# Optimization experiments

Measured on AMD Instinct MI355X. Metric: run time of the kernel, lower is better.

The kernel has to match this reference:

```python
import jax, jax.numpy as jnp
import numpy as np

N_NODES = 50000
N_EDGES = 1600000
IN_CH = 128
OUT_CH = 64
HEADS = 2
NEG_SLOPE = 0.2


def setup_inputs() -> dict:
    key = jax.random.key(0)
    ks = jax.random.split(key, 9)
    return {
        "x": jax.random.normal(ks[0], (N_NODES, IN_CH), dtype=jnp.float32),
        "embedding": jax.random.normal(ks[1], (N_NODES, OUT_CH), dtype=jnp.float32),
        "lin_w": jax.random.normal(ks[2], (IN_CH, HEADS * OUT_CH), dtype=jnp.float32) * (1.0 / np.sqrt(IN_CH)),
        "att_i": jax.random.normal(ks[3], (HEADS, OUT_CH), dtype=jnp.float32) * 0.1,
        "att_j": jax.random.normal(ks[4], (HEADS, OUT_CH), dtype=jnp.float32) * 0.1,
        "att_em_i": jax.random.normal(ks[5], (HEADS, OUT_CH), dtype=jnp.float32) * 0.1,
        "att_em_j": jax.random.normal(ks[6], (HEADS, OUT_CH), dtype=jnp.float32) * 0.1,
        "edge_src": jax.random.randint(ks[7], (N_EDGES,), 0, N_NODES, dtype=jnp.int64 if jax.config.read("jax_enable_x64") else jnp.int32),
        "edge_dst": jax.random.randint(ks[8], (N_EDGES,), 0, N_NODES, dtype=jnp.int64 if jax.config.read("jax_enable_x64") else jnp.int32),
    }


def reference(x, embedding, lin_w, att_i, att_j, att_em_i, att_em_j, edge_src, edge_dst):
    N = x.shape[0]
    H, D = att_i.shape
    # linear projection: [N, H, D]
    xh = (x @ lin_w).reshape(N, H, D)
    # add self loops
    loop = jnp.arange(N, dtype=edge_src.dtype)
    src = jnp.concatenate([edge_src, loop])
    dst = jnp.concatenate([edge_dst, loop])
    # per-node attention scores (cat(x, emb) . cat(att, att_em) split into two dots)
    s_i = jnp.einsum("nhd,hd->nh", xh, att_i) + embedding @ att_em_i.T  # [N,H]
    s_j = jnp.einsum("nhd,hd->nh", xh, att_j) + embedding @ att_em_j.T  # [N,H]
    # per-edge attention: x_i is src feature, x_j is dst feature (as in source)
    alpha = jax.nn.leaky_relu(s_i[src] + s_j[dst], negative_slope=NEG_SLOPE)  # [E+N,H]
    alpha = jax.nn.softmax(alpha, axis=1)  # softmax over heads, per the source code
    # message is alpha * x[dst]; aggregated at dst => x[n] * sum of alpha over incoming edges
    w = jax.ops.segment_sum(alpha, dst, num_segments=N)  # [N,H]
    out = xh * w[:, :, None]  # [N,H,D]
    return out.mean(axis=1)  # [N,D]
```

## Files before the change

### kernel.cpp

```cpp
#include <hip/hip_runtime.h>

#define IN_CH 128
#define OUT_CH 64
#define NEG_SLOPE 0.2f

#define CHUNK 2048
#define BSHIFT 10
#define SPLITS 6
#define CAPMAX 36864
#define FIX22 4194304.0f

typedef short bf16x8 __attribute__((ext_vector_type(8)));
typedef float f32x4 __attribute__((ext_vector_type(4)));
typedef unsigned long long u64;
typedef unsigned int u32;

__device__ __forceinline__ unsigned short f2bf(float f) {
  union { float f; unsigned u; } v;
  v.f = f;
  unsigned r = v.u + 0x7FFF + ((v.u >> 16) & 1);
  return (unsigned short)(r >> 16);
}

__global__ __launch_bounds__(256) void prep_kernel(
    const float* __restrict__ lw, const float* __restrict__ att_i,
    const float* __restrict__ att_j, unsigned short* __restrict__ lwt,
    float* __restrict__ u, int* __restrict__ gcur) {
  const int bid = blockIdx.x;
  const int tid = threadIdx.x;
  if (bid == 0) gcur[tid] = 0;
  if (bid < 64) {
    int idx = bid * 256 + tid;
    int k = idx >> 7;
    int c = idx & 127;
    lwt[(size_t)c * IN_CH + k] = f2bf(lw[idx]);
  } else {
    int which = bid - 64;
    const float* att = which ? att_j : att_i;
    int k = tid & 127;
    int h = (tid >> 7) & 1;
    float v = 0.f;
#pragma unroll 8
    for (int d = 0; d < 64; ++d)
      v = fmaf(lw[(size_t)k * IN_CH + h * 64 + d], att[h * 64 + d], v);
    u[which * 256 + h * 128 + k] = v;
  }
}

__global__ __launch_bounds__(256) void score_kernel(
    const float* __restrict__ x, const float* __restrict__ emb,
    const float* __restrict__ u, const float* __restrict__ aei,
    const float* __restrict__ aej, float2* __restrict__ si,
    float2* __restrict__ sj, float* __restrict__ wself,
    u64* __restrict__ wsum64, int N) {
  const int tid = threadIdx.x;
  const int wave = tid >> 6;
  const int lane = tid & 63;
  const int n = blockIdx.x * 4 + wave;
  if (n >= N) return;

  float x0 = x[(size_t)n * IN_CH + lane];
  float x1 = x[(size_t)n * IN_CH + 64 + lane];
  float em = emb[(size_t)n * OUT_CH + lane];

  float v_si0 = fmaf(x0, u[lane], fmaf(x1, u[64 + lane], em * aei[lane]));
  float v_si1 =
      fmaf(x0, u[128 + lane], fmaf(x1, u[192 + lane], em * aei[64 + lane]));
  float v_sj0 =
      fmaf(x0, u[256 + lane], fmaf(x1, u[320 + lane], em * aej[lane]));
  float v_sj1 =
      fmaf(x0, u[384 + lane], fmaf(x1, u[448 + lane], em * aej[64 + lane]));

#pragma unroll
  for (int off = 32; off > 0; off >>= 1) {
    v_si0 += __shfl_xor(v_si0, off, 64);
    v_si1 += __shfl_xor(v_si1, off, 64);
    v_sj0 += __shfl_xor(v_sj0, off, 64);
    v_sj1 += __shfl_xor(v_sj1, off, 64);
  }

  if (lane == 0) {
    si[n] = make_float2(v_si0, v_si1);
    sj[n] = make_float2(v_sj0, v_sj1);
    float a0 = v_si0 + v_sj0;
    float a1 = v_si1 + v_sj1;
    a0 = a0 > 0.f ? a0 : NEG_SLOPE * a0;
    a1 = a1 > 0.f ? a1 : NEG_SLOPE * a1;
    wself[n] = 1.f / (1.f + __expf(a1 - a0));
    wsum64[n] = 0ull;
  }
}

__global__ __launch_bounds__(256) void bin_kernel(
    const int* __restrict__ esrc, const int* __restrict__ edst,
    const float2* __restrict__ si, const float2* __restrict__ sj,
    u32* __restrict__ brecs, int* __restrict__ gcur,
    u64* __restrict__ wsum64, int cap, int E) {
  __shared__ u32 recs[CHUNK];
  __shared__ int hist[64];
  __shared__ int scan[64];
  __shared__ int gbase[64];
  __shared__ int cur[64];
  const int bid = blockIdx.x;
  const int tid = threadIdx.x;

  if (tid < 64) hist[tid] = 0;
  __syncthreads();

  const long e0 = (long)bid * CHUNK;
  const int cnt = (int)min((long)CHUNK, (long)E - e0);

  for (int r = tid; r < cnt; r += 256)
    atomicAdd(&hist[edst[e0 + r] >> BSHIFT], 1);
  __syncthreads();

  if (tid < 64) {
    int h = hist[tid];
    int v = h;
#pragma unroll
    for (int off = 1; off < 64; off <<= 1) {
      int t = __shfl_up(v, off, 64);
      if (tid >= off) v += t;
    }
    int excl = v - h;
    scan[tid] = excl;
    cur[tid] = excl;
    gbase[tid] = (h > 0) ? atomicAdd(&gcur[tid], h) : 0;
  }
  __syncthreads();

  for (int r = tid; r < cnt; r += 256) {
    long e = e0 + r;
    int s = esrc[e];
    int d = edst[e];
    float2 aa = si[s];
    float2 bb = sj[d];
    float a0 = aa.x + bb.x;
    float a1 = aa.y + bb.y;
    a0 = a0 > 0.f ? a0 : NEG_SLOPE * a0;
    a1 = a1 > 0.f ? a1 : NEG_SLOPE * a1;
    float p0 = 1.f / (1.f + __expf(a1 - a0));
    u32 fx = (u32)fminf(p0 * FIX22 + 0.5f, 4194303.0f);
    int pos = atomicAdd(&cur[d >> BSHIFT], 1);
    recs[pos] = ((u32)(d & 1023) << 22) | fx;
  }
  __syncthreads();

  for (int p = tid; p < cnt; p += 256) {
    int lo = 0, hi = 63;
#pragma unroll
    for (int it = 0; it < 6; ++it) {
      int mid = (lo + hi + 1) >> 1;
      if (scan[mid] <= p) lo = mid; else hi = mid - 1;
    }
    int b = lo;
    int gofs = gbase[b] + (p - scan[b]);
    u32 rec = recs[p];
    if (gofs < cap) {
      brecs[(size_t)b * cap + gofs] = rec;
    } else {
      atomicAdd(&wsum64[(b << BSHIFT) + (int)(rec >> 22)],
                (1ull << 32) | (u64)(rec & 0x3FFFFFu));
    }
  }
}

__global__ __launch_bounds__(256) void acc_kernel(
    const u32* __restrict__ brecs, const int* __restrict__ gcur,
    u64* __restrict__ ptabs, int cap) {
  __shared__ u64 tab[1024];
  const int bid = blockIdx.x;
  const int tid = threadIdx.x;
  const int p = bid / SPLITS;
  const int s = bid - p * SPLITS;

  for (int i = tid; i < 1024; i += 256) tab[i] = 0ull;
  __syncthreads();

  const int cnt = min(gcur[p], cap);
  const int per = (cnt + SPLITS - 1) / SPLITS;
  const int lo = s * per;
  const int hi = min(lo + per, cnt);
  const u32* rp = brecs + (size_t)p * cap;
  for (int r = lo + tid; r < hi; r += 256) {
    u32 rec = rp[r];
    atomicAdd(&tab[rec >> 22], (1ull << 32) | (u64)(rec & 0x3FFFFFu));
  }
  __syncthreads();

  u64* op = ptabs + ((size_t)bid << 10);
  for (int i = tid; i < 1024; i += 256) op[i] = tab[i];
}

__global__ __launch_bounds__(256) void gemm_out_kernel(
    const float* __restrict__ x, const unsigned short* __restrict__ lwt,
    const u64* __restrict__ wsum64, const u64* __restrict__ ptabs,
    const float* __restrict__ wself, float* __restrict__ out, int N) {
  const int tid = threadIdx.x;
  const int wave = tid >> 6;
  const int lane = tid & 63;
  const int ko = (lane >> 4) * 8;
  const int ccol = lane & 15;
  const int row0 = blockIdx.x * 64 + wave * 16;

  int arow = row0 + (lane & 15);
  if (arow >= N) arow = N - 1;
  const float* ap = x + (size_t)arow * IN_CH + ko;
  bf16x8 a[4];
#pragma unroll
  for (int kb = 0; kb < 4; ++kb) {
    float4 f0 = *(const float4*)(ap + kb * 32);
    float4 f1 = *(const float4*)(ap + kb * 32 + 4);
    bf16x8 t;
    t[0] = (short)f2bf(f0.x); t[1] = (short)f2bf(f0.y);
    t[2] = (short)f2bf(f0.z); t[3] = (short)f2bf(f0.w);
    t[4] = (short)f2bf(f1.x); t[5] = (short)f2bf(f1.y);
    t[6] = (short)f2bf(f1.z); t[7] = (short)f2bf(f1.w);
    a[kb] = t;
  }

  const int crow0 = row0 + (lane >> 4) * 4;
  float w0r[4], w1r[4];
#pragma unroll
  for (int rr = 0; rr < 4; ++rr) {
    int n = crow0 + rr;
    if (n >= N) n = N - 1;
    u64 acc = wsum64[n];
    const u64* pt = ptabs + (((size_t)(n >> BSHIFT) * SPLITS) << 10) + (n & 1023);
#pragma unroll
    for (int s5 = 0; s5 < SPLITS; ++s5) acc += pt[(size_t)s5 << 10];
    float cnt = (float)(u32)(acc >> 32);
    float s0 = (float)(u32)(acc & 0xFFFFFFFFu) * (1.0f / FIX22);
    float ps = wself[n];
    w0r[rr] = 0.5f * (s0 + ps);
    w1r[rr] = 0.5f * ((cnt - s0) + (1.f - ps));
  }

#pragma unroll
  for (int nt = 0; nt < 4; ++nt) {
    f32x4 acc0 = {0.f, 0.f, 0.f, 0.f};
    f32x4 acc1 = {0.f, 0.f, 0.f, 0.f};
    const bf16x8* bp0 =
        (const bf16x8*)(lwt + (size_t)(nt * 16 + ccol) * IN_CH + ko);
    const bf16x8* bp1 =
        (const bf16x8*)(lwt + (size_t)(64 + nt * 16 + ccol) * IN_CH + ko);
#pragma unroll
    for (int kb = 0; kb < 4; ++kb) {
      acc0 = __builtin_amdgcn_mfma_f32_16x16x32_bf16(a[kb], bp0[kb * 4], acc0,
                                                     0, 0, 0);
      acc1 = __builtin_amdgcn_mfma_f32_16x16x32_bf16(a[kb], bp1[kb * 4], acc1,
                                                     0, 0, 0);
    }
#pragma unroll
    for (int rr = 0; rr < 4; ++rr) {
      int n = crow0 + rr;
      if (n < N)
        out[(size_t)n * OUT_CH + nt * 16 + ccol] =
            fmaf(acc0[rr], w0r[rr], acc1[rr] * w1r[rr]);
    }
  }
}

extern "C" void kernel_launch(void* const* d_in, const int* in_sizes, int n_in,
                              void* d_out, int out_size, void* d_ws,
                              size_t ws_size, hipStream_t stream) {
  const float* x = (const float*)d_in[0];
  const float* emb = (const float*)d_in[1];
  const float* lw = (const float*)d_in[2];
  const float* att_i = (const float*)d_in[3];
  const float* att_j = (const float*)d_in[4];
  const float* aei = (const float*)d_in[5];
  const float* aej = (const float*)d_in[6];
  const int* esrc = (const int*)d_in[7];
  const int* edst = (const int*)d_in[8];
  float* out = (float*)d_out;

  int N = in_sizes[0] / IN_CH;
  int E = in_sizes[7];
  int nbkt = (N + 1023) >> BSHIFT;
  int nbin = (E + CHUNK - 1) / CHUNK;

  char* ws = (char*)d_ws;
  u64* wsum64 = (u64*)ws;
  u64* ptabs = wsum64 + N;
  float2* si = (float2*)(ptabs + (size_t)nbkt * SPLITS * 1024);
  float2* sj = si + N;
  float* wself = (float*)(sj + N);
  float* u = wself + N;
  unsigned short* lwt = (unsigned short*)(u + 512);
  int* gcur = (int*)(lwt + 16384);
  u32* brecs = (u32*)(gcur + 256);

  size_t fixed = (size_t)((char*)brecs - ws);
  size_t avail = ws_size > fixed ? (ws_size - fixed) / 4 : 0;
  int cap = (int)(avail / (nbkt > 0 ? nbkt : 1));
  if (cap > CAPMAX) cap = CAPMAX;
  if (cap < 4096) cap = 4096;

  prep_kernel<<<dim3(66), dim3(256), 0, stream>>>(lw, att_i, att_j, lwt, u,
                                                  gcur);
  score_kernel<<<dim3((N + 3) / 4), dim3(256), 0, stream>>>(
      x, emb, u, aei, aej, si, sj, wself, wsum64, N);
  bin_kernel<<<dim3(nbin), dim3(256), 0, stream>>>(esrc, edst, si, sj, brecs,
                                                   gcur, wsum64, cap, E);
  acc_kernel<<<dim3(nbkt * SPLITS), dim3(256), 0, stream>>>(brecs, gcur, ptabs,
                                                            cap);
  gemm_out_kernel<<<dim3((N + 63) / 64), dim3(256), 0, stream>>>(
      x, lwt, wsum64, ptabs, wself, out, N);
}
```

Baseline: 176.7 us.

## Overlap projection GEMM with edge binning and fuse accumulation into output pass

The projection GEMM now runs as extra blocks inside the binning kernel and writes bf16 projected features to a workspace buffer, so it overlaps with edge binning. The separate accumulation kernel and split partial tables are replaced by one reduce kernel per quarter-bucket. That kernel builds the per-node weight sums in shared memory and then scales the stored projections to produce the output, which removes one launch and the partial-table traffic. In exchange it writes and re-reads a bf16 intermediate of N×128, adds bf16 rounding of xh, and makes each of the four blocks per bucket scan all of that bucket's records.

```diff
diff --git a/kernel.cpp b/kernel.cpp
--- a/kernel.cpp
+++ b/kernel.cpp
@@ -6,7 +6,7 @@
 
 #define CHUNK 2048
 #define BSHIFT 10
-#define SPLITS 6
+#define NGEMM 391
 #define CAPMAX 36864
 #define FIX22 4194304.0f
 
@@ -20,6 +20,12 @@
   v.f = f;
   unsigned r = v.u + 0x7FFF + ((v.u >> 16) & 1);
   return (unsigned short)(r >> 16);
+}
+
+__device__ __forceinline__ float bf2f(unsigned short h) {
+  union { unsigned u; float f; } v;
+  v.u = (unsigned)h << 16;
+  return v.f;
 }
 
 __global__ __launch_bounds__(256) void prep_kernel(
@@ -91,11 +97,13 @@
   }
 }
 
-__global__ __launch_bounds__(256) void bin_kernel(
+__global__ __launch_bounds__(256) void bin_gemm_kernel(
+    const float* __restrict__ x, const unsigned short* __restrict__ lwt,
     const int* __restrict__ esrc, const int* __restrict__ edst,
     const float2* __restrict__ si, const float2* __restrict__ sj,
-    u32* __restrict__ brecs, int* __restrict__ gcur,
-    u64* __restrict__ wsum64, int cap, int E) {
+    unsigned short* __restrict__ xhb, u64* __restrict__ wsum64,
+    u32* __restrict__ brecs, int* __restrict__ gcur, int cap, int nbin, int N,
+    int E) {
   __shared__ u32 recs[CHUNK];
   __shared__ int hist[64];
   __shared__ int scan[64];
@@ -103,161 +111,154 @@
   __shared__ int cur[64];
   const int bid = blockIdx.x;
   const int tid = threadIdx.x;
-
-  if (tid < 64) hist[tid] = 0;
-  __syncthreads();
-
-  const long e0 = (long)bid * CHUNK;
-  const int cnt = (int)min((long)CHUNK, (long)E - e0);
-
-  for (int r = tid; r < cnt; r += 256)
-    atomicAdd(&hist[edst[e0 + r] >> BSHIFT], 1);
-  __syncthreads();
-
-  if (tid < 64) {
-    int h = hist[tid];
-    int v = h;
-#pragma unroll
-    for (int off = 1; off < 64; off <<= 1) {
-      int t = __shfl_up(v, off, 64);
-      if (tid >= off) v += t;
-    }
-    int excl = v - h;
-    scan[tid] = excl;
-    cur[tid] = excl;
-    gbase[tid] = (h > 0) ? atomicAdd(&gcur[tid], h) : 0;
-  }
-  __syncthreads();
-
-  for (int r = tid; r < cnt; r += 256) {
-    long e = e0 + r;
-    int s = esrc[e];
-    int d = edst[e];
-    float2 aa = si[s];
-    float2 bb = sj[d];
-    float a0 = aa.x + bb.x;
-    float a1 = aa.y + bb.y;
-    a0 = a0 > 0.f ? a0 : NEG_SLOPE * a0;
-    a1 = a1 > 0.f ? a1 : NEG_SLOPE * a1;
-    float p0 = 1.f / (1.f + __expf(a1 - a0));
-    u32 fx = (u32)fminf(p0 * FIX22 + 0.5f, 4194303.0f);
-    int pos = atomicAdd(&cur[d >> BSHIFT], 1);
-    recs[pos] = ((u32)(d & 1023) << 22) | fx;
-  }
-  __syncthreads();
-
-  for (int p = tid; p < cnt; p += 256) {
-    int lo = 0, hi = 63;
-#pragma unroll
-    for (int it = 0; it < 6; ++it) {
-      int mid = (lo + hi + 1) >> 1;
-      if (scan[mid] <= p) lo = mid; else hi = mid - 1;
-    }
-    int b = lo;
-    int gofs = gbase[b] + (p - scan[b]);
-    u32 rec = recs[p];
-    if (gofs < cap) {
-      brecs[(size_t)b * cap + gofs] = rec;
-    } else {
-      atomicAdd(&wsum64[(b << BSHIFT) + (int)(rec >> 22)],
-                (1ull << 32) | (u64)(rec & 0x3FFFFFu));
-    }
-  }
-}
-
-__global__ __launch_bounds__(256) void acc_kernel(
-    const u32* __restrict__ brecs, const int* __restrict__ gcur,
-    u64* __restrict__ ptabs, int cap) {
-  __shared__ u64 tab[1024];
-  const int bid = blockIdx.x;
-  const int tid = threadIdx.x;
-  const int p = bid / SPLITS;
-  const int s = bid - p * SPLITS;
-
-  for (int i = tid; i < 1024; i += 256) tab[i] = 0ull;
-  __syncthreads();
-
-  const int cnt = min(gcur[p], cap);
-  const int per = (cnt + SPLITS - 1) / SPLITS;
-  const int lo = s * per;
-  const int hi = min(lo + per, cnt);
-  const u32* rp = brecs + (size_t)p * cap;
-  for (int r = lo + tid; r < hi; r += 256) {
-    u32 rec = rp[r];
-    atomicAdd(&tab[rec >> 22], (1ull << 32) | (u64)(rec & 0x3FFFFFu));
-  }
-  __syncthreads();
-
-  u64* op = ptabs + ((size_t)bid << 10);
-  for (int i = tid; i < 1024; i += 256) op[i] = tab[i];
-}
-
-__global__ __launch_bounds__(256) void gemm_out_kernel(
-    const float* __restrict__ x, const unsigned short* __restrict__ lwt,
-    const u64* __restrict__ wsum64, const u64* __restrict__ ptabs,
-    const float* __restrict__ wself, float* __restrict__ out, int N) {
-  const int tid = threadIdx.x;
   const int wave = tid >> 6;
   const int lane = tid & 63;
-  const int ko = (lane >> 4) * 8;
-  const int ccol = lane & 15;
-  const int row0 = blockIdx.x * 64 + wave * 16;
-
-  int arow = row0 + (lane & 15);
-  if (arow >= N) arow = N - 1;
-  const float* ap = x + (size_t)arow * IN_CH + ko;
-  bf16x8 a[4];
-#pragma unroll
-  for (int kb = 0; kb < 4; ++kb) {
-    float4 f0 = *(const float4*)(ap + kb * 32);
-    float4 f1 = *(const float4*)(ap + kb * 32 + 4);
-    bf16x8 t;
-    t[0] = (short)f2bf(f0.x); t[1] = (short)f2bf(f0.y);
-    t[2] = (short)f2bf(f0.z); t[3] = (short)f2bf(f0.w);
-    t[4] = (short)f2bf(f1.x); t[5] = (short)f2bf(f1.y);
-    t[6] = (short)f2bf(f1.z); t[7] = (short)f2bf(f1.w);
-    a[kb] = t;
-  }
-
-  const int crow0 = row0 + (lane >> 4) * 4;
-  float w0r[4], w1r[4];
-#pragma unroll
-  for (int rr = 0; rr < 4; ++rr) {
-    int n = crow0 + rr;
-    if (n >= N) n = N - 1;
-    u64 acc = wsum64[n];
-    const u64* pt = ptabs + (((size_t)(n >> BSHIFT) * SPLITS) << 10) + (n & 1023);
-#pragma unroll
-    for (int s5 = 0; s5 < SPLITS; ++s5) acc += pt[(size_t)s5 << 10];
-    float cnt = (float)(u32)(acc >> 32);
+
+  if (bid < nbin) {
+    if (tid < 64) hist[tid] = 0;
+    __syncthreads();
+
+    const long e0 = (long)bid * CHUNK;
+    const int cnt = (int)min((long)CHUNK, (long)E - e0);
+
+    for (int r = tid; r < cnt; r += 256)
+      atomicAdd(&hist[edst[e0 + r] >> BSHIFT], 1);
+    __syncthreads();
+
+    if (tid < 64) {
+      int h = hist[tid];
+      int v = h;
+#pragma unroll
+      for (int off = 1; off < 64; off <<= 1) {
+        int t = __shfl_up(v, off, 64);
+        if (tid >= off) v += t;
+      }
+      int excl = v - h;
+      scan[tid] = excl;
+      cur[tid] = excl;
+      gbase[tid] = (h > 0) ? atomicAdd(&gcur[tid], h) : 0;
+    }
+    __syncthreads();
+
+    for (int r = tid; r < cnt; r += 256) {
+      long e = e0 + r;
+      int s = esrc[e];
+      int d = edst[e];
+      float2 aa = si[s];
+      float2 bb = sj[d];
+      float a0 = aa.x + bb.x;
+      float a1 = aa.y + bb.y;
+      a0 = a0 > 0.f ? a0 : NEG_SLOPE * a0;
+      a1 = a1 > 0.f ? a1 : NEG_SLOPE * a1;
+      float p0 = 1.f / (1.f + __expf(a1 - a0));
+      u32 fx = (u32)fminf(p0 * FIX22 + 0.5f, 4194303.0f);
+      int pos = atomicAdd(&cur[d >> BSHIFT], 1);
+      recs[pos] = ((u32)(d & 1023) << 22) | fx;
+    }
+    __syncthreads();
+
+    for (int p = tid; p < cnt; p += 256) {
+      int lo = 0, hi = 63;
+#pragma unroll
+      for (int it = 0; it < 6; ++it) {
+        int mid = (lo + hi + 1) >> 1;
+        if (scan[mid] <= p) lo = mid; else hi = mid - 1;
+      }
+      int b = lo;
+      int gofs = gbase[b] + (p - scan[b]);
+      u32 rec = recs[p];
+      if (gofs < cap) {
+        brecs[(size_t)b * cap + gofs] = rec;
+      } else {
+        atomicAdd(&wsum64[(b << BSHIFT) + (int)(rec >> 22)],
+                  (1ull << 32) | (u64)(rec & 0x3FFFFFu));
+      }
+    }
+  } else {
+    const int g = bid - nbin;
+    const int ntiles = (N + 63) / 64;
+    const int ko = (lane >> 4) * 8;
+    const int ccol = lane & 15;
+    for (int tile = g; tile < ntiles; tile += NGEMM) {
+      const int row0 = tile * 64 + wave * 16;
+      int arow = row0 + (lane & 15);
+      if (arow >= N) arow = N - 1;
+      const float* ap = x + (size_t)arow * IN_CH + ko;
+      bf16x8 a[4];
+#pragma unroll
+      for (int kb = 0; kb < 4; ++kb) {
+        float4 f0 = *(const float4*)(ap + kb * 32);
+        float4 f1 = *(const float4*)(ap + kb * 32 + 4);
+        bf16x8 t;
+        t[0] = (short)f2bf(f0.x); t[1] = (short)f2bf(f0.y);
+        t[2] = (short)f2bf(f0.z); t[3] = (short)f2bf(f0.w);
+        t[4] = (short)f2bf(f1.x); t[5] = (short)f2bf(f1.y);
+        t[6] = (short)f2bf(f1.z); t[7] = (short)f2bf(f1.w);
+        a[kb] = t;
+      }
+      const int crow0 = row0 + (lane >> 4) * 4;
+#pragma unroll
+      for (int nt = 0; nt < 8; ++nt) {
+        f32x4 acc = {0.f, 0.f, 0.f, 0.f};
+        const bf16x8* bp =
+            (const bf16x8*)(lwt + (size_t)(nt * 16 + ccol) * IN_CH + ko);
+        acc = __builtin_amdgcn_mfma_f32_16x16x32_bf16(a[0], bp[0], acc, 0, 0, 0);
+        acc = __builtin_amdgcn_mfma_f32_16x16x32_bf16(a[1], bp[4], acc, 0, 0, 0);
+        acc = __builtin_amdgcn_mfma_f32_16x16x32_bf16(a[2], bp[8], acc, 0, 0, 0);
+        acc = __builtin_amdgcn_mfma_f32_16x16x32_bf16(a[3], bp[12], acc, 0, 0, 0);
+#pragma unroll
+        for (int rr = 0; rr < 4; ++rr) {
+          int n = crow0 + rr;
+          if (n < N) xhb[(size_t)n * IN_CH + nt * 16 + ccol] = f2bf(acc[rr]);
+        }
+      }
+    }
+  }
+}
+
+__global__ __launch_bounds__(1024) void reduce_out_kernel(
+    const unsigned short* __restrict__ xhb, const u64* __restrict__ wsum64,
+    const float* __restrict__ wself, const u32* __restrict__ brecs,
+    const int* __restrict__ gcur, int cap, float* __restrict__ out, int N) {
+  __shared__ u64 tab[256];
+  const int bid = blockIdx.x;
+  const int p = bid >> 2;
+  const int q = bid & 3;
+  const int tid = threadIdx.x;
+
+  if (tid < 256) tab[tid] = 0ull;
+  __syncthreads();
+
+  const int cnt = min(gcur[p], cap);
+  const u32* rp = brecs + (size_t)p * cap;
+  for (int r = tid; r < cnt; r += 1024) {
+    u32 rec = rp[r];
+    if ((int)(rec >> 30) == q)
+      atomicAdd(&tab[(rec >> 22) & 255], (1ull << 32) | (u64)(rec & 0x3FFFFFu));
+  }
+  __syncthreads();
+
+  const int n0 = (p << BSHIFT) + (q << 8);
+  const int nmax = min(256, N - n0);
+  if (nmax <= 0) return;
+  for (int t = tid; t < nmax * 16; t += 1024) {
+    int ln = t >> 4;
+    int n = n0 + ln;
+    int c4 = (t & 15) << 2;
+    u64 acc = tab[ln] + wsum64[n];
+    float cnt_f = (float)(u32)(acc >> 32);
     float s0 = (float)(u32)(acc & 0xFFFFFFFFu) * (1.0f / FIX22);
     float ps = wself[n];
-    w0r[rr] = 0.5f * (s0 + ps);
-    w1r[rr] = 0.5f * ((cnt - s0) + (1.f - ps));
-  }
-
-#pragma unroll
-  for (int nt = 0; nt < 4; ++nt) {
-    f32x4 acc0 = {0.f, 0.f, 0.f, 0.f};
-    f32x4 acc1 = {0.f, 0.f, 0.f, 0.f};
-    const bf16x8* bp0 =
-        (const bf16x8*)(lwt + (size_t)(nt * 16 + ccol) * IN_CH + ko);
-    const bf16x8* bp1 =
-        (const bf16x8*)(lwt + (size_t)(64 + nt * 16 + ccol) * IN_CH + ko);
-#pragma unroll
-    for (int kb = 0; kb < 4; ++kb) {
-      acc0 = __builtin_amdgcn_mfma_f32_16x16x32_bf16(a[kb], bp0[kb * 4], acc0,
-                                                     0, 0, 0);
-      acc1 = __builtin_amdgcn_mfma_f32_16x16x32_bf16(a[kb], bp1[kb * 4], acc1,
-                                                     0, 0, 0);
-    }
-#pragma unroll
-    for (int rr = 0; rr < 4; ++rr) {
-      int n = crow0 + rr;
-      if (n < N)
-        out[(size_t)n * OUT_CH + nt * 16 + ccol] =
-            fmaf(acc0[rr], w0r[rr], acc1[rr] * w1r[rr]);
-    }
+    float w0 = 0.5f * (s0 + ps);
+    float w1 = 0.5f * ((cnt_f - s0) + (1.f - ps));
+    ushort4 h0 = *(const ushort4*)&xhb[(size_t)n * IN_CH + c4];
+    ushort4 h1 = *(const ushort4*)&xhb[(size_t)n * IN_CH + 64 + c4];
+    float4 o;
+    o.x = fmaf(bf2f(h0.x), w0, bf2f(h1.x) * w1);
+    o.y = fmaf(bf2f(h0.y), w0, bf2f(h1.y) * w1);
+    o.z = fmaf(bf2f(h0.z), w0, bf2f(h1.z) * w1);
+    o.w = fmaf(bf2f(h0.w), w0, bf2f(h1.w) * w1);
+    *(float4*)&out[(size_t)n * OUT_CH + c4] = o;
   }
 }
 
@@ -282,13 +283,13 @@
 
   char* ws = (char*)d_ws;
   u64* wsum64 = (u64*)ws;
-  u64* ptabs = wsum64 + N;
-  float2* si = (float2*)(ptabs + (size_t)nbkt * SPLITS * 1024);
+  float2* si = (float2*)(wsum64 + N);
   float2* sj = si + N;
   float* wself = (float*)(sj + N);
   float* u = wself + N;
   unsigned short* lwt = (unsigned short*)(u + 512);
-  int* gcur = (int*)(lwt + 16384);
+  unsigned short* xhb = lwt + 16384;
+  int* gcur = (int*)(xhb + (size_t)N * IN_CH);
   u32* brecs = (u32*)(gcur + 256);
 
   size_t fixed = (size_t)((char*)brecs - ws);
@@ -301,10 +302,8 @@
                                                   gcur);
   score_kernel<<<dim3((N + 3) / 4), dim3(256), 0, stream>>>(
       x, emb, u, aei, aej, si, sj, wself, wsum64, N);
-  bin_kernel<<<dim3(nbin), dim3(256), 0, stream>>>(esrc, edst, si, sj, brecs,
-                                                   gcur, wsum64, cap, E);
-  acc_kernel<<<dim3(nbkt * SPLITS), dim3(256), 0, stream>>>(brecs, gcur, ptabs,
-                                                            cap);
-  gemm_out_kernel<<<dim3((N + 63) / 64), dim3(256), 0, stream>>>(
-      x, lwt, wsum64, ptabs, wself, out, N);
-}
+  bin_gemm_kernel<<<dim3(nbin + NGEMM), dim3(256), 0, stream>>>(
+      x, lwt, esrc, edst, si, sj, xhb, wsum64, brecs, gcur, cap, nbin, N, E);
+  reduce_out_kernel<<<dim3(nbkt * 4), dim3(1024), 0, stream>>>(
+      xhb, wsum64, wself, brecs, gcur, cap, out, N);
+}
```

Result: faster. 171.5 us (-3.0%).
